# Kernel optimization log

Measured on AMD Instinct MI355X. Metric: run time of the kernel, lower is better.

The kernel has to match this reference:

```python
import jax, jax.numpy as jnp
import numpy as np

EPS = 1e-8

def setup_inputs() -> dict:
    key = jax.random.key(0)
    k1, k2, k3 = jax.random.split(key, 3)
    B, N, M = 4, 8192, 8192
    source = jax.random.normal(k1, (B, N, 3), dtype=jnp.float32)
    target = jax.random.normal(k2, (B, M, 3), dtype=jnp.float32)
    weights = jax.random.uniform(k3, (B, N), dtype=jnp.float32)
    return {"source": source, "target": target, "weights": weights}

def reference(source, target, weights):
    # Pairwise squared distances: (B, N, M)
    diff = source[:, :, None, :] - target[:, None, :, :]
    sq_distances = jnp.sum(diff * diff, axis=-1)
    # squared=False -> take sqrt with eps for stability
    distances = jnp.sqrt(sq_distances + EPS)
    # source -> target nearest-neighbor distance, weighted
    s2t = jnp.min(distances, axis=2) * weights  # (B, N)
    forward_loss = jnp.mean(s2t)
    # symmetric=True: target -> source (unweighted, as in original)
    t2s = jnp.min(distances, axis=1)  # (B, M)
    backward_loss = jnp.mean(t2s)
    return forward_loss + backward_loss
```

## Files before the change

### kernel.cpp

```cpp
#include <hip/hip_runtime.h>
#include <math.h>


#define EPS 1e-8f

typedef _Float16 f16x8 __attribute__((ext_vector_type(8)));
typedef float    f32x16 __attribute__((ext_vector_type(16)));

constexpr int B_    = 4;
constexpr int N_    = 8192;
constexpr int TPB   = 256;
constexpr int QPW   = 64;
constexpr int QPB   = 4 * QPW;
constexpr int RCH   = 8;
constexpr int CHUNK = N_ / RCH;
constexpr int RB    = 64;
constexpr unsigned int INF_BITS = 0x7F7FFFFFu;

__global__ __launch_bounds__(TPB)
void prep_kernel(const float* __restrict__ src, const float* __restrict__ tgt,
                 f16x8* __restrict__ srcA, f16x8* __restrict__ srcB, float* __restrict__ srcS,
                 f16x8* __restrict__ tgtA, f16x8* __restrict__ tgtB, float* __restrict__ tgtS,
                 unsigned int* __restrict__ minA, unsigned int* __restrict__ minB,
                 float* __restrict__ out)
{
    const _Float16 h0 = (_Float16)0.f;
    const _Float16 h1 = (_Float16)1.f;
    int t = blockIdx.x * TPB + threadIdx.x;
    {
        const float* p = src + (size_t)t * 3;
        _Float16 hx = (_Float16)p[0], hy = (_Float16)p[1], hz = (_Float16)p[2];
        float fx = (float)hx, fy = (float)hy, fz = (float)hz;
        float rsq = fx * fx + fy * fy + fz * fz;
        _Float16 rh = (_Float16)rsq;
        _Float16 rl = (_Float16)(rsq - (float)rh);
        f16x8 a = {(_Float16)(-2.f * fx), (_Float16)(-2.f * fy),
                   (_Float16)(-2.f * fz), rh, rl, h0, h0, h0};
        f16x8 bq = {hx, hy, hz, h1, h1, h0, h0, h0};
        srcA[t] = a; srcB[t] = bq; srcS[t] = rsq;
    }
    {
        const float* p = tgt + (size_t)t * 3;
        _Float16 hx = (_Float16)p[0], hy = (_Float16)p[1], hz = (_Float16)p[2];
        float fx = (float)hx, fy = (float)hy, fz = (float)hz;
        float rsq = fx * fx + fy * fy + fz * fz;
        _Float16 rh = (_Float16)rsq;
        _Float16 rl = (_Float16)(rsq - (float)rh);
        f16x8 a = {(_Float16)(-2.f * fx), (_Float16)(-2.f * fy),
                   (_Float16)(-2.f * fz), rh, rl, h0, h0, h0};
        f16x8 bq = {hx, hy, hz, h1, h1, h0, h0, h0};
        tgtA[t] = a; tgtB[t] = bq; tgtS[t] = rsq;
    }
    minA[t] = INF_BITS;
    minB[t] = INF_BITS;
    if (t == 0) out[0] = 0.f;
}

__global__ __launch_bounds__(TPB)
void nn_mfma_kernel(const f16x8* __restrict__ srcA, const f16x8* __restrict__ srcB,
                    const float* __restrict__ srcS,
                    const f16x8* __restrict__ tgtA, const f16x8* __restrict__ tgtB,
                    const float* __restrict__ tgtS,
                    unsigned int* __restrict__ minA, unsigned int* __restrict__ minB)
{
    __shared__ f16x8 sref[CHUNK + 1];

    const int zb  = blockIdx.z;
    const int dir = zb >> 2;
    const int b   = zb & 3;
    const f16x8* Ap = (dir ? srcA : tgtA) + (size_t)b * N_ + (size_t)blockIdx.y * CHUNK;
    const f16x8* Bp = (dir ? tgtB : srcB) + (size_t)b * N_;
    const float* Sp = (dir ? tgtS : srcS) + (size_t)b * N_;
    unsigned int* omin = (dir ? minB : minA) + (size_t)b * N_;

    const int tid = threadIdx.x;
    for (int k = tid; k < CHUNK; k += TPB) sref[k] = Ap[k];
    if (tid == 0) {
        f16x8 z = {(_Float16)0.f, (_Float16)0.f, (_Float16)0.f, (_Float16)0.f,
                   (_Float16)0.f, (_Float16)0.f, (_Float16)0.f, (_Float16)0.f};
        sref[CHUNK] = z;
    }

    const int lane = tid & 63;
    const int wv   = tid >> 6;
    const int l31  = lane & 31;
    const int half = lane >> 5;
    const int qb   = blockIdx.x * QPB + wv * QPW;

    f16x8 B0 = {(_Float16)0.f, (_Float16)0.f, (_Float16)0.f, (_Float16)0.f,
                (_Float16)0.f, (_Float16)0.f, (_Float16)0.f, (_Float16)0.f};
    f16x8 B1 = B0;
    float qs0 = 0.f, qs1 = 0.f;
    if (half == 0) {
        B0  = Bp[qb + l31];
        B1  = Bp[qb + 32 + l31];
        qs0 = Sp[qb + l31];
        qs1 = Sp[qb + 32 + l31];
    }
    __syncthreads();

    f32x16 zc;
#pragma unroll
    for (int i = 0; i < 16; ++i) zc[i] = 0.f;

    int idx = (half == 0) ? l31 : CHUNK;
    const int step = (half == 0) ? 32 : 0;
    float mn0 = 3.0e38f, mn1 = 3.0e38f;

    for (int s = 0; s < CHUNK / 32; ++s) {
        f16x8 a = sref[idx];
        idx += step;
        f32x16 d0 = __builtin_amdgcn_mfma_f32_32x32x16_f16(a, B0, zc, 0, 0, 0);
        f32x16 d1 = __builtin_amdgcn_mfma_f32_32x32x16_f16(a, B1, zc, 0, 0, 0);
#pragma unroll
        for (int r = 0; r < 16; r += 2) {
            mn0 = fminf(fminf(d0[r], d0[r + 1]), mn0);
            mn1 = fminf(fminf(d1[r], d1[r + 1]), mn1);
        }
    }

    mn0 = fminf(mn0, __shfl_xor(mn0, 32));
    mn1 = fminf(mn1, __shfl_xor(mn1, 32));
    if (half == 0) {
        atomicMin(&omin[qb + l31],      __float_as_uint(fmaxf(mn0 + qs0, 0.f)));
        atomicMin(&omin[qb + 32 + l31], __float_as_uint(fmaxf(mn1 + qs1, 0.f)));
    }
}

__global__ __launch_bounds__(TPB)
void reduce_kernel(const unsigned int* __restrict__ minA,
                   const unsigned int* __restrict__ minB,
                   const float* __restrict__ w,
                   float* __restrict__ out)
{
    const int BN = B_ * N_;
    const float invBN = 1.0f / (float)BN;

    float sum = 0.0f;
    for (int t = blockIdx.x * TPB + threadIdx.x; t < BN; t += RB * TPB) {
        sum += sqrtf(__uint_as_float(minA[t]) + EPS) * w[t];
        sum += sqrtf(__uint_as_float(minB[t]) + EPS);
    }
    sum *= invBN;

    __shared__ float ss[TPB / 64];
    int lane = threadIdx.x & 63;
    int wid  = threadIdx.x >> 6;
#pragma unroll
    for (int off = 32; off > 0; off >>= 1) sum += __shfl_down(sum, off);
    if (lane == 0) ss[wid] = sum;
    __syncthreads();
    if (threadIdx.x == 0) {
        float s = 0.0f;
#pragma unroll
        for (int i = 0; i < TPB / 64; ++i) s += ss[i];
        atomicAdd(out, s);
    }
}

extern "C" void kernel_launch(void* const* d_in, const int* in_sizes, int n_in,
                              void* d_out, int out_size, void* d_ws, size_t ws_size,
                              hipStream_t stream)
{
    const float* src = (const float*)d_in[0];
    const float* tgt = (const float*)d_in[1];
    const float* w   = (const float*)d_in[2];
    float* out = (float*)d_out;

    const size_t BN = (size_t)B_ * N_;
    char* p = (char*)d_ws;
    f16x8* srcA = (f16x8*)p;            p += BN * sizeof(f16x8);
    f16x8* srcB = (f16x8*)p;            p += BN * sizeof(f16x8);
    f16x8* tgtA = (f16x8*)p;            p += BN * sizeof(f16x8);
    f16x8* tgtB = (f16x8*)p;            p += BN * sizeof(f16x8);
    float* srcS = (float*)p;            p += BN * sizeof(float);
    float* tgtS = (float*)p;            p += BN * sizeof(float);
    unsigned int* minA = (unsigned int*)p;  p += BN * sizeof(unsigned int);
    unsigned int* minB = (unsigned int*)p;

    prep_kernel<<<BN / TPB, TPB, 0, stream>>>(src, tgt, srcA, srcB, srcS,
                                              tgtA, tgtB, tgtS, minA, minB, out);

    dim3 grid(N_ / QPB, RCH, 2 * B_);
    nn_mfma_kernel<<<grid, TPB, 0, stream>>>(srcA, srcB, srcS,
                                             tgtA, tgtB, tgtS, minA, minB);

    reduce_kernel<<<RB, TPB, 0, stream>>>(minA, minB, w, out);
}
```

Baseline: 83.59 us.

## Fuse fp16 operand prep into NN kernel and replace prep with memsets

Removes the separate prep kernel. The MFMA kernel now converts raw float3 points to fp16 operand vectors on the fly, both the reference chunk into shared memory and the query B operands into registers, and the min buffers and output are initialised with hipMemsetAsync. It also software-prefetches the next shared-memory operand, splits the min reduction into two independent accumulator chains, and sets a launch bound of 6 blocks. The goal is to drop a kernel launch and the workspace round trip, at the cost of redundant conversion work in every block and strided 12-byte global loads.

Result: faster. 76.75 us (-8.2%).

```diff
diff --git a/kernel.cpp b/kernel.cpp
--- a/kernel.cpp
+++ b/kernel.cpp
@@ -15,70 +15,38 @@
 constexpr int RCH   = 8;
 constexpr int CHUNK = N_ / RCH;
 constexpr int RB    = 64;
-constexpr unsigned int INF_BITS = 0x7F7FFFFFu;
 
-__global__ __launch_bounds__(TPB)
-void prep_kernel(const float* __restrict__ src, const float* __restrict__ tgt,
-                 f16x8* __restrict__ srcA, f16x8* __restrict__ srcB, float* __restrict__ srcS,
-                 f16x8* __restrict__ tgtA, f16x8* __restrict__ tgtB, float* __restrict__ tgtS,
-                 unsigned int* __restrict__ minA, unsigned int* __restrict__ minB,
-                 float* __restrict__ out)
+__global__ __launch_bounds__(TPB, 6)
+void nn_mfma_kernel(const float* __restrict__ src, const float* __restrict__ tgt,
+                    unsigned int* __restrict__ minA, unsigned int* __restrict__ minB)
 {
+    __shared__ f16x8 sref[CHUNK + 64];
+
+    const int zb  = blockIdx.z;
+    const int dir = zb >> 2;
+    const int b   = zb & 3;
+    const float* Rraw = (dir ? src : tgt) + ((size_t)b * N_ + (size_t)blockIdx.y * CHUNK) * 3;
+    const float* Qraw = (dir ? tgt : src) + (size_t)b * N_ * 3;
+    unsigned int* omin = (dir ? minB : minA) + (size_t)b * N_;
+
+    const int tid = threadIdx.x;
     const _Float16 h0 = (_Float16)0.f;
     const _Float16 h1 = (_Float16)1.f;
-    int t = blockIdx.x * TPB + threadIdx.x;
-    {
-        const float* p = src + (size_t)t * 3;
-        _Float16 hx = (_Float16)p[0], hy = (_Float16)p[1], hz = (_Float16)p[2];
+
+    for (int k = tid; k < CHUNK; k += TPB) {
+        const float* rp = Rraw + (size_t)k * 3;
+        _Float16 hx = (_Float16)rp[0], hy = (_Float16)rp[1], hz = (_Float16)rp[2];
         float fx = (float)hx, fy = (float)hy, fz = (float)hz;
         float rsq = fx * fx + fy * fy + fz * fz;
         _Float16 rh = (_Float16)rsq;
         _Float16 rl = (_Float16)(rsq - (float)rh);
         f16x8 a = {(_Float16)(-2.f * fx), (_Float16)(-2.f * fy),
                    (_Float16)(-2.f * fz), rh, rl, h0, h0, h0};
-        f16x8 bq = {hx, hy, hz, h1, h1, h0, h0, h0};
-        srcA[t] = a; srcB[t] = bq; srcS[t] = rsq;
+        sref[k] = a;
     }
-    {
-        const float* p = tgt + (size_t)t * 3;
-        _Float16 hx = (_Float16)p[0], hy = (_Float16)p[1], hz = (_Float16)p[2];
-        float fx = (float)hx, fy = (float)hy, fz = (float)hz;
-        float rsq = fx * fx + fy * fy + fz * fz;
-        _Float16 rh = (_Float16)rsq;
-        _Float16 rl = (_Float16)(rsq - (float)rh);
-        f16x8 a = {(_Float16)(-2.f * fx), (_Float16)(-2.f * fy),
-                   (_Float16)(-2.f * fz), rh, rl, h0, h0, h0};
-        f16x8 bq = {hx, hy, hz, h1, h1, h0, h0, h0};
-        tgtA[t] = a; tgtB[t] = bq; tgtS[t] = rsq;
-    }
-    minA[t] = INF_BITS;
-    minB[t] = INF_BITS;
-    if (t == 0) out[0] = 0.f;
-}
-
-__global__ __launch_bounds__(TPB)
-void nn_mfma_kernel(const f16x8* __restrict__ srcA, const f16x8* __restrict__ srcB,
-                    const float* __restrict__ srcS,
-                    const f16x8* __restrict__ tgtA, const f16x8* __restrict__ tgtB,
-                    const float* __restrict__ tgtS,
-                    unsigned int* __restrict__ minA, unsigned int* __restrict__ minB)
-{
-    __shared__ f16x8 sref[CHUNK + 1];
-
-    const int zb  = blockIdx.z;
-    const int dir = zb >> 2;
-    const int b   = zb & 3;
-    const f16x8* Ap = (dir ? srcA : tgtA) + (size_t)b * N_ + (size_t)blockIdx.y * CHUNK;
-    const f16x8* Bp = (dir ? tgtB : srcB) + (size_t)b * N_;
-    const float* Sp = (dir ? tgtS : srcS) + (size_t)b * N_;
-    unsigned int* omin = (dir ? minB : minA) + (size_t)b * N_;
-
-    const int tid = threadIdx.x;
-    for (int k = tid; k < CHUNK; k += TPB) sref[k] = Ap[k];
-    if (tid == 0) {
-        f16x8 z = {(_Float16)0.f, (_Float16)0.f, (_Float16)0.f, (_Float16)0.f,
-                   (_Float16)0.f, (_Float16)0.f, (_Float16)0.f, (_Float16)0.f};
-        sref[CHUNK] = z;
+    if (tid < 64) {
+        f16x8 z = {h0, h0, h0, h0, h0, h0, h0, h0};
+        sref[CHUNK + tid] = z;
     }
 
     const int lane = tid & 63;
@@ -87,15 +55,20 @@
     const int half = lane >> 5;
     const int qb   = blockIdx.x * QPB + wv * QPW;
 
-    f16x8 B0 = {(_Float16)0.f, (_Float16)0.f, (_Float16)0.f, (_Float16)0.f,
-                (_Float16)0.f, (_Float16)0.f, (_Float16)0.f, (_Float16)0.f};
+    f16x8 B0 = {h0, h0, h0, h0, h0, h0, h0, h0};
     f16x8 B1 = B0;
     float qs0 = 0.f, qs1 = 0.f;
     if (half == 0) {
-        B0  = Bp[qb + l31];
-        B1  = Bp[qb + 32 + l31];
-        qs0 = Sp[qb + l31];
-        qs1 = Sp[qb + 32 + l31];
+        const float* q0 = Qraw + (size_t)(qb + l31) * 3;
+        const float* q1 = Qraw + (size_t)(qb + 32 + l31) * 3;
+        _Float16 ax = (_Float16)q0[0], ay = (_Float16)q0[1], az = (_Float16)q0[2];
+        _Float16 bx = (_Float16)q1[0], by = (_Float16)q1[1], bz = (_Float16)q1[2];
+        float fax = (float)ax, fay = (float)ay, faz = (float)az;
+        float fbx = (float)bx, fby = (float)by, fbz = (float)bz;
+        B0 = f16x8{ax, ay, az, h1, h1, h0, h0, h0};
+        B1 = f16x8{bx, by, bz, h1, h1, h0, h0, h0};
+        qs0 = fax * fax + fay * fay + faz * faz;
+        qs1 = fbx * fbx + fby * fby + fbz * fbz;
     }
     __syncthreads();
 
@@ -105,20 +78,30 @@
 
     int idx = (half == 0) ? l31 : CHUNK;
     const int step = (half == 0) ? 32 : 0;
-    float mn0 = 3.0e38f, mn1 = 3.0e38f;
+    float mn0a = 3.0e38f, mn0b = 3.0e38f, mn1a = 3.0e38f, mn1b = 3.0e38f;
 
+    f16x8 a = sref[idx];
+    idx += step;
     for (int s = 0; s < CHUNK / 32; ++s) {
-        f16x8 a = sref[idx];
+        f16x8 an = sref[idx];
         idx += step;
         f32x16 d0 = __builtin_amdgcn_mfma_f32_32x32x16_f16(a, B0, zc, 0, 0, 0);
         f32x16 d1 = __builtin_amdgcn_mfma_f32_32x32x16_f16(a, B1, zc, 0, 0, 0);
 #pragma unroll
-        for (int r = 0; r < 16; r += 2) {
-            mn0 = fminf(fminf(d0[r], d0[r + 1]), mn0);
-            mn1 = fminf(fminf(d1[r], d1[r + 1]), mn1);
+        for (int r = 0; r < 8; r += 2) {
+            mn0a = fminf(fminf(d0[r], d0[r + 1]), mn0a);
+            mn1a = fminf(fminf(d1[r], d1[r + 1]), mn1a);
         }
+#pragma unroll
+        for (int r = 8; r < 16; r += 2) {
+            mn0b = fminf(fminf(d0[r], d0[r + 1]), mn0b);
+            mn1b = fminf(fminf(d1[r], d1[r + 1]), mn1b);
+        }
+        a = an;
     }
 
+    float mn0 = fminf(mn0a, mn0b);
+    float mn1 = fminf(mn1a, mn1b);
     mn0 = fminf(mn0, __shfl_xor(mn0, 32));
     mn1 = fminf(mn1, __shfl_xor(mn1, 32));
     if (half == 0) {
@@ -168,22 +151,14 @@
     float* out = (float*)d_out;
 
     const size_t BN = (size_t)B_ * N_;
-    char* p = (char*)d_ws;
-    f16x8* srcA = (f16x8*)p;            p += BN * sizeof(f16x8);
-    f16x8* srcB = (f16x8*)p;            p += BN * sizeof(f16x8);
-    f16x8* tgtA = (f16x8*)p;            p += BN * sizeof(f16x8);
-    f16x8* tgtB = (f16x8*)p;            p += BN * sizeof(f16x8);
-    float* srcS = (float*)p;            p += BN * sizeof(float);
-    float* tgtS = (float*)p;            p += BN * sizeof(float);
-    unsigned int* minA = (unsigned int*)p;  p += BN * sizeof(unsigned int);
-    unsigned int* minB = (unsigned int*)p;
+    unsigned int* minA = (unsigned int*)d_ws;
+    unsigned int* minB = minA + BN;
 
-    prep_kernel<<<BN / TPB, TPB, 0, stream>>>(src, tgt, srcA, srcB, srcS,
-                                              tgtA, tgtB, tgtS, minA, minB, out);
+    hipMemsetAsync(minA, 0x7F, 2 * BN * sizeof(unsigned int), stream);
+    hipMemsetAsync(out, 0, sizeof(float), stream);
 
     dim3 grid(N_ / QPB, RCH, 2 * B_);
-    nn_mfma_kernel<<<grid, TPB, 0, stream>>>(srcA, srcB, srcS,
-                                             tgtA, tgtB, tgtS, minA, minB);
+    nn_mfma_kernel<<<grid, TPB, 0, stream>>>(src, tgt, minA, minB);
 
     reduce_kernel<<<RB, TPB, 0, stream>>>(minA, minB, w, out);
 }
```

## Hold reference chunk in registers, write per-chunk partial minima, drop atomics

Applied to the files above, without the earlier changes.

The NN kernel now splits the reference set into 32 chunks of 256, so each lane holds its 8 A fragments in registers instead of staging them in LDS. MFMA issue is software-pipelined against the min-folds, and each fold uses two accumulators. Atomic mins are replaced by plain stores of per-chunk partial minima, which the reduce kernel combines; this also removes the min-buffer init from prep. In exchange the grid has 4x more blocks, B fragments are reloaded 4x more often, and the reduce reads a 32x larger partial buffer (about 8 MB).

Measured after the change: 80.78 us. 1.03x faster.

```diff
diff --git a/kernel.cpp b/kernel.cpp
--- a/kernel.cpp
+++ b/kernel.cpp
@@ -12,16 +12,23 @@
 constexpr int TPB   = 256;
 constexpr int QPW   = 64;
 constexpr int QPB   = 4 * QPW;
-constexpr int RCH   = 8;
+constexpr int RCH   = 32;
 constexpr int CHUNK = N_ / RCH;
-constexpr int RB    = 64;
-constexpr unsigned int INF_BITS = 0x7F7FFFFFu;
+constexpr int NF    = CHUNK / 32;
+constexpr int RB    = 128;
+
+#define FOLD(d, ma, mb)                                         \
+    _Pragma("unroll")                                           \
+    for (int r = 0; r < 8; r += 2)                              \
+        ma = fminf(fminf(d[r], d[r + 1]), ma);                  \
+    _Pragma("unroll")                                           \
+    for (int r = 8; r < 16; r += 2)                             \
+        mb = fminf(fminf(d[r], d[r + 1]), mb);
 
 __global__ __launch_bounds__(TPB)
 void prep_kernel(const float* __restrict__ src, const float* __restrict__ tgt,
                  f16x8* __restrict__ srcA, f16x8* __restrict__ srcB, float* __restrict__ srcS,
                  f16x8* __restrict__ tgtA, f16x8* __restrict__ tgtB, float* __restrict__ tgtS,
-                 unsigned int* __restrict__ minA, unsigned int* __restrict__ minB,
                  float* __restrict__ out)
 {
     const _Float16 h0 = (_Float16)0.f;
@@ -34,10 +41,10 @@
         float rsq = fx * fx + fy * fy + fz * fz;
         _Float16 rh = (_Float16)rsq;
         _Float16 rl = (_Float16)(rsq - (float)rh);
-        f16x8 a = {(_Float16)(-2.f * fx), (_Float16)(-2.f * fy),
-                   (_Float16)(-2.f * fz), rh, rl, h0, h0, h0};
-        f16x8 bq = {hx, hy, hz, h1, h1, h0, h0, h0};
-        srcA[t] = a; srcB[t] = bq; srcS[t] = rsq;
+        srcA[t] = f16x8{(_Float16)(-2.f * fx), (_Float16)(-2.f * fy),
+                        (_Float16)(-2.f * fz), rh, rl, h0, h0, h0};
+        srcB[t] = f16x8{hx, hy, hz, h1, h1, h0, h0, h0};
+        srcS[t] = rsq;
     }
     {
         const float* p = tgt + (size_t)t * 3;
@@ -46,100 +53,98 @@
         float rsq = fx * fx + fy * fy + fz * fz;
         _Float16 rh = (_Float16)rsq;
         _Float16 rl = (_Float16)(rsq - (float)rh);
-        f16x8 a = {(_Float16)(-2.f * fx), (_Float16)(-2.f * fy),
-                   (_Float16)(-2.f * fz), rh, rl, h0, h0, h0};
-        f16x8 bq = {hx, hy, hz, h1, h1, h0, h0, h0};
-        tgtA[t] = a; tgtB[t] = bq; tgtS[t] = rsq;
+        tgtA[t] = f16x8{(_Float16)(-2.f * fx), (_Float16)(-2.f * fy),
+                        (_Float16)(-2.f * fz), rh, rl, h0, h0, h0};
+        tgtB[t] = f16x8{hx, hy, hz, h1, h1, h0, h0, h0};
+        tgtS[t] = rsq;
     }
-    minA[t] = INF_BITS;
-    minB[t] = INF_BITS;
     if (t == 0) out[0] = 0.f;
 }
 
-__global__ __launch_bounds__(TPB)
-void nn_mfma_kernel(const f16x8* __restrict__ srcA, const f16x8* __restrict__ srcB,
-                    const float* __restrict__ srcS,
-                    const f16x8* __restrict__ tgtA, const f16x8* __restrict__ tgtB,
-                    const float* __restrict__ tgtS,
-                    unsigned int* __restrict__ minA, unsigned int* __restrict__ minB)
+__global__ __launch_bounds__(TPB, 4)
+void nn_reg_kernel(const f16x8* __restrict__ srcA, const f16x8* __restrict__ srcB,
+                   const float* __restrict__ srcS,
+                   const f16x8* __restrict__ tgtA, const f16x8* __restrict__ tgtB,
+                   const float* __restrict__ tgtS,
+                   float* __restrict__ part)
 {
-    __shared__ f16x8 sref[CHUNK + 1];
-
     const int zb  = blockIdx.z;
     const int dir = zb >> 2;
     const int b   = zb & 3;
     const f16x8* Ap = (dir ? srcA : tgtA) + (size_t)b * N_ + (size_t)blockIdx.y * CHUNK;
     const f16x8* Bp = (dir ? tgtB : srcB) + (size_t)b * N_;
     const float* Sp = (dir ? tgtS : srcS) + (size_t)b * N_;
-    unsigned int* omin = (dir ? minB : minA) + (size_t)b * N_;
+    float* opart = part + ((size_t)zb * RCH + blockIdx.y) * N_;
 
-    const int tid = threadIdx.x;
-    for (int k = tid; k < CHUNK; k += TPB) sref[k] = Ap[k];
-    if (tid == 0) {
-        f16x8 z = {(_Float16)0.f, (_Float16)0.f, (_Float16)0.f, (_Float16)0.f,
-                   (_Float16)0.f, (_Float16)0.f, (_Float16)0.f, (_Float16)0.f};
-        sref[CHUNK] = z;
-    }
-
+    const int tid  = threadIdx.x;
     const int lane = tid & 63;
     const int wv   = tid >> 6;
     const int l31  = lane & 31;
     const int half = lane >> 5;
     const int qb   = blockIdx.x * QPB + wv * QPW;
 
-    f16x8 B0 = {(_Float16)0.f, (_Float16)0.f, (_Float16)0.f, (_Float16)0.f,
-                (_Float16)0.f, (_Float16)0.f, (_Float16)0.f, (_Float16)0.f};
-    f16x8 B1 = B0;
+    const _Float16 h0 = (_Float16)0.f;
+    const f16x8 zf = {h0, h0, h0, h0, h0, h0, h0, h0};
+
+    f16x8 B0 = zf, B1 = zf;
     float qs0 = 0.f, qs1 = 0.f;
+    f16x8 A[NF];
+#pragma unroll
+    for (int u = 0; u < NF; ++u) A[u] = zf;
     if (half == 0) {
         B0  = Bp[qb + l31];
         B1  = Bp[qb + 32 + l31];
         qs0 = Sp[qb + l31];
         qs1 = Sp[qb + 32 + l31];
-    }
-    __syncthreads();
-
-    f32x16 zc;
 #pragma unroll
-    for (int i = 0; i < 16; ++i) zc[i] = 0.f;
-
-    int idx = (half == 0) ? l31 : CHUNK;
-    const int step = (half == 0) ? 32 : 0;
-    float mn0 = 3.0e38f, mn1 = 3.0e38f;
-
-    for (int s = 0; s < CHUNK / 32; ++s) {
-        f16x8 a = sref[idx];
-        idx += step;
-        f32x16 d0 = __builtin_amdgcn_mfma_f32_32x32x16_f16(a, B0, zc, 0, 0, 0);
-        f32x16 d1 = __builtin_amdgcn_mfma_f32_32x32x16_f16(a, B1, zc, 0, 0, 0);
-#pragma unroll
-        for (int r = 0; r < 16; r += 2) {
-            mn0 = fminf(fminf(d0[r], d0[r + 1]), mn0);
-            mn1 = fminf(fminf(d1[r], d1[r + 1]), mn1);
-        }
+        for (int u = 0; u < NF; ++u) A[u] = Ap[u * 32 + l31];
     }
 
+    const f32x16 zc = {};
+    float mn0a = 3.0e38f, mn0b = 3.0e38f, mn1a = 3.0e38f, mn1b = 3.0e38f;
+
+    f32x16 dA0 = __builtin_amdgcn_mfma_f32_32x32x16_f16(A[0], B0, zc, 0, 0, 0);
+    f32x16 dA1 = __builtin_amdgcn_mfma_f32_32x32x16_f16(A[0], B1, zc, 0, 0, 0);
+#pragma unroll
+    for (int u = 1; u < NF; ++u) {
+        f32x16 dB0 = __builtin_amdgcn_mfma_f32_32x32x16_f16(A[u], B0, zc, 0, 0, 0);
+        FOLD(dA0, mn0a, mn0b)
+        f32x16 dB1 = __builtin_amdgcn_mfma_f32_32x32x16_f16(A[u], B1, zc, 0, 0, 0);
+        FOLD(dA1, mn1a, mn1b)
+        dA0 = dB0;
+        dA1 = dB1;
+    }
+    FOLD(dA0, mn0a, mn0b)
+    FOLD(dA1, mn1a, mn1b)
+
+    float mn0 = fminf(mn0a, mn0b);
+    float mn1 = fminf(mn1a, mn1b);
     mn0 = fminf(mn0, __shfl_xor(mn0, 32));
     mn1 = fminf(mn1, __shfl_xor(mn1, 32));
     if (half == 0) {
-        atomicMin(&omin[qb + l31],      __float_as_uint(fmaxf(mn0 + qs0, 0.f)));
-        atomicMin(&omin[qb + 32 + l31], __float_as_uint(fmaxf(mn1 + qs1, 0.f)));
+        opart[qb + l31]      = fmaxf(mn0 + qs0, 0.f);
+        opart[qb + 32 + l31] = fmaxf(mn1 + qs1, 0.f);
     }
 }
 
 __global__ __launch_bounds__(TPB)
-void reduce_kernel(const unsigned int* __restrict__ minA,
-                   const unsigned int* __restrict__ minB,
+void reduce_kernel(const float* __restrict__ part,
                    const float* __restrict__ w,
                    float* __restrict__ out)
 {
-    const int BN = B_ * N_;
-    const float invBN = 1.0f / (float)BN;
+    const int Q = 2 * B_ * N_;
+    const float invBN = 1.0f / (float)(B_ * N_);
 
     float sum = 0.0f;
-    for (int t = blockIdx.x * TPB + threadIdx.x; t < BN; t += RB * TPB) {
-        sum += sqrtf(__uint_as_float(minA[t]) + EPS) * w[t];
-        sum += sqrtf(__uint_as_float(minB[t]) + EPS);
+    for (int t = blockIdx.x * TPB + threadIdx.x; t < Q; t += RB * TPB) {
+        const int zb = t >> 13;
+        const int qn = t & (N_ - 1);
+        const float* p = part + ((size_t)zb * RCH) * N_ + qn;
+        float m = p[0];
+#pragma unroll
+        for (int c = 1; c < RCH; ++c) m = fminf(m, p[(size_t)c * N_]);
+        float d = sqrtf(m + EPS);
+        sum += (zb < 4) ? d * w[(size_t)zb * N_ + qn] : d;
     }
     sum *= invBN;
 
@@ -175,15 +180,14 @@
     f16x8* tgtB = (f16x8*)p;            p += BN * sizeof(f16x8);
     float* srcS = (float*)p;            p += BN * sizeof(float);
     float* tgtS = (float*)p;            p += BN * sizeof(float);
-    unsigned int* minA = (unsigned int*)p;  p += BN * sizeof(unsigned int);
-    unsigned int* minB = (unsigned int*)p;
+    float* part = (float*)p;
 
     prep_kernel<<<BN / TPB, TPB, 0, stream>>>(src, tgt, srcA, srcB, srcS,
-                                              tgtA, tgtB, tgtS, minA, minB, out);
+                                              tgtA, tgtB, tgtS, out);
 
     dim3 grid(N_ / QPB, RCH, 2 * B_);
-    nn_mfma_kernel<<<grid, TPB, 0, stream>>>(srcA, srcB, srcS,
-                                             tgtA, tgtB, tgtS, minA, minB);
+    nn_reg_kernel<<<grid, TPB, 0, stream>>>(srcA, srcB, srcS,
+                                            tgtA, tgtB, tgtS, part);
 
-    reduce_kernel<<<RB, TPB, 0, stream>>>(minA, minB, w, out);
+    reduce_kernel<<<RB, TPB, 0, stream>>>(part, w, out);
 }
```
